# Optimization experiments

Hardware: AMD Instinct MI355X
Metric: run time of the kernel (lower is better)

Reference implementation:

```python
import jax, jax.numpy as jnp
import numpy as np

NORM_EPS = 1e-6


def setup_inputs() -> dict:
    key = jax.random.key(0)
    k1, k2 = jax.random.split(key)
    in_features, out_features = 4096, 4096
    x = jax.random.normal(k1, (2, 2048, in_features), dtype=jnp.float32)
    scale = 1.0 / np.sqrt(in_features)
    weight = jax.random.normal(k2, (out_features, in_features), dtype=jnp.float32) * scale
    norm_weight = jnp.ones((in_features,), dtype=jnp.float32)
    return {"x": x, "weight": weight, "norm_weight": norm_weight}


def reference(x, weight, norm_weight):
    # RMSNorm over the last dim
    rms = jnp.sqrt(jnp.mean(x * x, axis=-1, keepdims=True) + NORM_EPS)
    x_n = x / rms * norm_weight
    # ternary weight quantization (absmean scale alpha)
    alpha = jnp.maximum(jnp.mean(jnp.abs(weight)), 1e-10)
    w_q = jnp.clip(jnp.round(weight / alpha), -1.0, 1.0)
    # per-token int8 activation quantization (absmax scale gamma)
    gamma = jnp.maximum(jnp.max(jnp.abs(x_n), axis=-1, keepdims=True), 1e-10)
    x_q = jnp.clip(jnp.round(x_n * 127.0 / gamma), -128.0, 127.0)
    # rescaled matmul: y = x_q @ w_q.T * (alpha * gamma / 127)
    y = jnp.einsum('bsk,nk->bsn', x_q, w_q) * (alpha * gamma / 127.0)
    return y
```

## Files before the change

### kernel.cpp

```cpp
#include <hip/hip_runtime.h>
#include <cstdint>
#include <cstddef>


#define KD 4096
#define MD 4096
#define ND 4096

typedef int i32x4 __attribute__((ext_vector_type(4)));

__device__ __forceinline__ void gl2lds16(const signed char* g, signed char* l) {
  __builtin_amdgcn_global_load_lds(
      (const __attribute__((address_space(1))) void*)g,
      (__attribute__((address_space(3))) void*)l, 16, 0, 0);
}

__device__ __forceinline__ float wave_sum(float v) {
#pragma unroll
  for (int off = 32; off; off >>= 1) v += __shfl_down(v, off, 64);
  return v;
}
__device__ __forceinline__ float wave_max(float v) {
#pragma unroll
  for (int off = 32; off; off >>= 1) v = fmaxf(v, __shfl_down(v, off, 64));
  return v;
}


__global__ __launch_bounds__(256) void k_alpha_part(const float* __restrict__ w,
                                                    float* __restrict__ part) {
  __shared__ float red[4];
  const int tid = threadIdx.x;
  const float4* w4 = (const float4*)(w + (size_t)blockIdx.x * 4096);
  float s = 0.f;
#pragma unroll
  for (int i = 0; i < 4; ++i) {
    float4 v = w4[i * 256 + tid];
    s += fabsf(v.x) + fabsf(v.y) + fabsf(v.z) + fabsf(v.w);
  }
  s = wave_sum(s);
  if ((tid & 63) == 0) red[tid >> 6] = s;
  __syncthreads();
  if (tid == 0) part[blockIdx.x] = (red[0] + red[1]) + (red[2] + red[3]);
}

__global__ __launch_bounds__(256) void k_alpha_final(const float* __restrict__ part,
                                                     float* __restrict__ alpha) {
  __shared__ float red[4];
  const int tid = threadIdx.x;
  float s = 0.f;
#pragma unroll
  for (int i = 0; i < 16; ++i) s += part[i * 256 + tid];
  s = wave_sum(s);
  if ((tid & 63) == 0) red[tid >> 6] = s;
  __syncthreads();
  if (tid == 0)
    alpha[0] = fmaxf(((red[0] + red[1]) + (red[2] + red[3])) * (1.0f / 16777216.0f),
                     1e-10f);
}


__global__ __launch_bounds__(256) void k_quant_w(const float* __restrict__ w,
                                                 const float* __restrict__ alpha_p,
                                                 signed char* __restrict__ wq) {
  const float alpha = alpha_p[0];
  const int tid = threadIdx.x;
  const float4* w4 = (const float4*)(w + (size_t)blockIdx.x * 4096);
  uint32_t* wqi = (uint32_t*)(wq + (size_t)blockIdx.x * 4096);
#pragma unroll
  for (int i = 0; i < 4; ++i) {
    const int f = i * 256 + tid;
    float4 v = w4[f];
    int q0 = (int)fminf(fmaxf(rintf(v.x / alpha), -1.f), 1.f);
    int q1 = (int)fminf(fmaxf(rintf(v.y / alpha), -1.f), 1.f);
    int q2 = (int)fminf(fmaxf(rintf(v.z / alpha), -1.f), 1.f);
    int q3 = (int)fminf(fmaxf(rintf(v.w / alpha), -1.f), 1.f);
    wqi[f] = (uint32_t)(q0 & 255) | ((uint32_t)(q1 & 255) << 8) |
             ((uint32_t)(q2 & 255) << 16) | ((uint32_t)(q3 & 255) << 24);
  }
}


__global__ __launch_bounds__(256) void k_rmsnorm_quant(const float* __restrict__ x,
                                                       const float* __restrict__ nw,
                                                       signed char* __restrict__ xq,
                                                       float* __restrict__ gamma) {
  __shared__ float red[4];
  __shared__ float red2[4];
  const int tid = threadIdx.x;
  const int row = blockIdx.x;
  const float4* x4 = (const float4*)(x + (size_t)row * 4096);
  const float4* n4 = (const float4*)nw;
  float4 xv[4], nv[4];
  float ss = 0.f;
#pragma unroll
  for (int i = 0; i < 4; ++i) {
    xv[i] = x4[i * 256 + tid];
    nv[i] = n4[i * 256 + tid];
    ss += xv[i].x * xv[i].x + xv[i].y * xv[i].y + xv[i].z * xv[i].z + xv[i].w * xv[i].w;
  }
  ss = wave_sum(ss);
  if ((tid & 63) == 0) red[tid >> 6] = ss;
  __syncthreads();
  const float tot = (red[0] + red[1]) + (red[2] + red[3]);
  const float rms = sqrtf(tot * (1.0f / 4096.0f) + 1e-6f);

  float4 xn[4];
  float mx = 0.f;
#pragma unroll
  for (int i = 0; i < 4; ++i) {
    xn[i].x = xv[i].x / rms * nv[i].x;
    xn[i].y = xv[i].y / rms * nv[i].y;
    xn[i].z = xv[i].z / rms * nv[i].z;
    xn[i].w = xv[i].w / rms * nv[i].w;
    mx = fmaxf(mx, fmaxf(fmaxf(fabsf(xn[i].x), fabsf(xn[i].y)),
                         fmaxf(fabsf(xn[i].z), fabsf(xn[i].w))));
  }
  mx = wave_max(mx);
  if ((tid & 63) == 0) red2[tid >> 6] = mx;
  __syncthreads();
  const float g = fmaxf(fmaxf(fmaxf(red2[0], red2[1]), fmaxf(red2[2], red2[3])),
                        1e-10f);
  if (tid == 0) gamma[row] = g;

  uint32_t* xqi = (uint32_t*)(xq + (size_t)row * 4096);
#pragma unroll
  for (int i = 0; i < 4; ++i) {
    const int f = i * 256 + tid;
    int q0 = (int)fminf(fmaxf(rintf(xn[i].x * 127.0f / g), -128.f), 127.f);
    int q1 = (int)fminf(fmaxf(rintf(xn[i].y * 127.0f / g), -128.f), 127.f);
    int q2 = (int)fminf(fmaxf(rintf(xn[i].z * 127.0f / g), -128.f), 127.f);
    int q3 = (int)fminf(fmaxf(rintf(xn[i].w * 127.0f / g), -128.f), 127.f);
    xqi[f] = (uint32_t)(q0 & 255) | ((uint32_t)(q1 & 255) << 8) |
             ((uint32_t)(q2 & 255) << 16) | ((uint32_t)(q3 & 255) << 24);
  }
}


__global__ __launch_bounds__(256) void k_gemm(const signed char* __restrict__ xq,
                                              const signed char* __restrict__ wq,
                                              const float* __restrict__ gamma,
                                              const float* __restrict__ alpha_p,
                                              float* __restrict__ out) {
  __shared__ __align__(16) signed char As[128 * 64];
  __shared__ __align__(16) signed char Bs[128 * 64];
  const int tid = threadIdx.x;
  const int lane = tid & 63;
  const int wave = tid >> 6;
  const int wm = (wave >> 1) * 64;
  const int wn = (wave & 1) * 64;
  const int quad = lane >> 4;
  const int l16 = lane & 15;
  const int bm = blockIdx.y * 128;
  const int bn = blockIdx.x * 128;

  const signed char* Ag = xq + (size_t)bm * KD;
  const signed char* Bg = wq + (size_t)bn * KD;

  const int srow = wave * 16 + (lane >> 2);
  const int schunk = (lane & 3) ^ ((lane >> 3) & 3);
  const signed char* agp0 = Ag + (size_t)srow * KD + schunk * 16;
  const signed char* agp1 = Ag + (size_t)(srow + 64) * KD + schunk * 16;
  const signed char* bgp0 = Bg + (size_t)srow * KD + schunk * 16;
  const signed char* bgp1 = Bg + (size_t)(srow + 64) * KD + schunk * 16;
  signed char* la0 = &As[wave * 1024];
  signed char* la1 = &As[4096 + wave * 1024];
  signed char* lb0 = &Bs[wave * 1024];
  signed char* lb1 = &Bs[4096 + wave * 1024];

  i32x4 acc[4][4];
#pragma unroll
  for (int i = 0; i < 4; ++i)
#pragma unroll
    for (int j = 0; j < 4; ++j) acc[i][j] = (i32x4){0, 0, 0, 0};

  const int sw = (l16 >> 1) & 3;
  const int apos = (quad ^ sw) * 16;

  for (int k0 = 0; k0 < KD; k0 += 64) {
    __syncthreads();
    gl2lds16(agp0 + k0, la0);
    gl2lds16(agp1 + k0, la1);
    gl2lds16(bgp0 + k0, lb0);
    gl2lds16(bgp1 + k0, lb1);
    __syncthreads();

    i32x4 af[4], bf[4];
#pragma unroll
    for (int mi = 0; mi < 4; ++mi)
      af[mi] = *(const i32x4*)&As[(wm + mi * 16 + l16) * 64 + apos];
#pragma unroll
    for (int ni = 0; ni < 4; ++ni)
      bf[ni] = *(const i32x4*)&Bs[(wn + ni * 16 + l16) * 64 + apos];
#pragma unroll
    for (int mi = 0; mi < 4; ++mi)
#pragma unroll
      for (int ni = 0; ni < 4; ++ni)
        acc[mi][ni] = __builtin_amdgcn_mfma_i32_16x16x64_i8(af[mi], bf[ni],
                                                            acc[mi][ni], 0, 0, 0);
  }

  const float alpha = alpha_p[0];
#pragma unroll
  for (int mi = 0; mi < 4; ++mi) {
#pragma unroll
    for (int r = 0; r < 4; ++r) {
      const int m = bm + wm + mi * 16 + quad * 4 + r;
      const float s = (alpha * gamma[m]) / 127.0f;
#pragma unroll
      for (int ni = 0; ni < 4; ++ni) {
        const int n = bn + wn + ni * 16 + l16;
        out[(size_t)m * ND + n] = (float)acc[mi][ni][r] * s;
      }
    }
  }
}


extern "C" void kernel_launch(void* const* d_in, const int* in_sizes, int n_in,
                              void* d_out, int out_size, void* d_ws, size_t ws_size,
                              hipStream_t stream) {
  const float* x = (const float*)d_in[0];
  const float* w = (const float*)d_in[1];
  const float* nw = (const float*)d_in[2];
  float* out = (float*)d_out;

  char* ws = (char*)d_ws;
  signed char* xq = (signed char*)ws;
  signed char* wq = (signed char*)(ws + ((size_t)1 << 24));
  float* gamma = (float*)(ws + ((size_t)2 << 24));
  float* part = (float*)(ws + ((size_t)2 << 24) + 16384);
  float* alpha = (float*)(ws + ((size_t)2 << 24) + 32768);

  k_alpha_part<<<4096, 256, 0, stream>>>(w, part);
  k_alpha_final<<<1, 256, 0, stream>>>(part, alpha);
  k_quant_w<<<4096, 256, 0, stream>>>(w, alpha, wq);
  k_rmsnorm_quant<<<4096, 256, 0, stream>>>(x, nw, xq, gamma);
  dim3 g(ND / 128, MD / 128);
  k_gemm<<<g, 256, 0, stream>>>(xq, wq, gamma, alpha, out);
}
```

Measured before the change: 269.9 us.

## Fuse alpha finalize and quantize kernels; double GEMM K-tile to 128

Merges the alpha-final, weight-quantize and RMSNorm-quantize kernels into one launch. Each weight block recomputes alpha from the partial sums, and activation rows are handled by the upper half of the grid. This removes two launches and the serial single-block kernel. The GEMM K step grows from 64 to 128 with a new XOR swizzle, halving the barrier-bounded iterations at the cost of doubling LDS per block to 32KB and redundantly reading the partials in every weight block.

```diff
diff --git a/kernel.cpp b/kernel.cpp
--- a/kernel.cpp
+++ b/kernel.cpp
@@ -44,95 +44,93 @@
   if (tid == 0) part[blockIdx.x] = (red[0] + red[1]) + (red[2] + red[3]);
 }
 
-__global__ __launch_bounds__(256) void k_alpha_final(const float* __restrict__ part,
-                                                     float* __restrict__ alpha) {
-  __shared__ float red[4];
+
+__global__ __launch_bounds__(256) void k_quant_all(const float* __restrict__ w,
+                                                   const float* __restrict__ x,
+                                                   const float* __restrict__ nw,
+                                                   const float* __restrict__ part,
+                                                   signed char* __restrict__ wq,
+                                                   signed char* __restrict__ xq,
+                                                   float* __restrict__ gamma,
+                                                   float* __restrict__ alpha_out) {
   const int tid = threadIdx.x;
-  float s = 0.f;
-#pragma unroll
-  for (int i = 0; i < 16; ++i) s += part[i * 256 + tid];
-  s = wave_sum(s);
-  if ((tid & 63) == 0) red[tid >> 6] = s;
-  __syncthreads();
-  if (tid == 0)
-    alpha[0] = fmaxf(((red[0] + red[1]) + (red[2] + red[3])) * (1.0f / 16777216.0f),
-                     1e-10f);
-}
-
-
-__global__ __launch_bounds__(256) void k_quant_w(const float* __restrict__ w,
-                                                 const float* __restrict__ alpha_p,
-                                                 signed char* __restrict__ wq) {
-  const float alpha = alpha_p[0];
-  const int tid = threadIdx.x;
-  const float4* w4 = (const float4*)(w + (size_t)blockIdx.x * 4096);
-  uint32_t* wqi = (uint32_t*)(wq + (size_t)blockIdx.x * 4096);
-#pragma unroll
-  for (int i = 0; i < 4; ++i) {
-    const int f = i * 256 + tid;
-    float4 v = w4[f];
-    int q0 = (int)fminf(fmaxf(rintf(v.x / alpha), -1.f), 1.f);
-    int q1 = (int)fminf(fmaxf(rintf(v.y / alpha), -1.f), 1.f);
-    int q2 = (int)fminf(fmaxf(rintf(v.z / alpha), -1.f), 1.f);
-    int q3 = (int)fminf(fmaxf(rintf(v.w / alpha), -1.f), 1.f);
-    wqi[f] = (uint32_t)(q0 & 255) | ((uint32_t)(q1 & 255) << 8) |
-             ((uint32_t)(q2 & 255) << 16) | ((uint32_t)(q3 & 255) << 24);
-  }
-}
-
-
-__global__ __launch_bounds__(256) void k_rmsnorm_quant(const float* __restrict__ x,
-                                                       const float* __restrict__ nw,
-                                                       signed char* __restrict__ xq,
-                                                       float* __restrict__ gamma) {
+  const int bid = blockIdx.x;
   __shared__ float red[4];
   __shared__ float red2[4];
-  const int tid = threadIdx.x;
-  const int row = blockIdx.x;
-  const float4* x4 = (const float4*)(x + (size_t)row * 4096);
-  const float4* n4 = (const float4*)nw;
-  float4 xv[4], nv[4];
-  float ss = 0.f;
-#pragma unroll
-  for (int i = 0; i < 4; ++i) {
-    xv[i] = x4[i * 256 + tid];
-    nv[i] = n4[i * 256 + tid];
-    ss += xv[i].x * xv[i].x + xv[i].y * xv[i].y + xv[i].z * xv[i].z + xv[i].w * xv[i].w;
-  }
-  ss = wave_sum(ss);
-  if ((tid & 63) == 0) red[tid >> 6] = ss;
-  __syncthreads();
-  const float tot = (red[0] + red[1]) + (red[2] + red[3]);
-  const float rms = sqrtf(tot * (1.0f / 4096.0f) + 1e-6f);
-
-  float4 xn[4];
-  float mx = 0.f;
-#pragma unroll
-  for (int i = 0; i < 4; ++i) {
-    xn[i].x = xv[i].x / rms * nv[i].x;
-    xn[i].y = xv[i].y / rms * nv[i].y;
-    xn[i].z = xv[i].z / rms * nv[i].z;
-    xn[i].w = xv[i].w / rms * nv[i].w;
-    mx = fmaxf(mx, fmaxf(fmaxf(fabsf(xn[i].x), fabsf(xn[i].y)),
-                         fmaxf(fabsf(xn[i].z), fabsf(xn[i].w))));
-  }
-  mx = wave_max(mx);
-  if ((tid & 63) == 0) red2[tid >> 6] = mx;
-  __syncthreads();
-  const float g = fmaxf(fmaxf(fmaxf(red2[0], red2[1]), fmaxf(red2[2], red2[3])),
-                        1e-10f);
-  if (tid == 0) gamma[row] = g;
-
-  uint32_t* xqi = (uint32_t*)(xq + (size_t)row * 4096);
-#pragma unroll
-  for (int i = 0; i < 4; ++i) {
-    const int f = i * 256 + tid;
-    int q0 = (int)fminf(fmaxf(rintf(xn[i].x * 127.0f / g), -128.f), 127.f);
-    int q1 = (int)fminf(fmaxf(rintf(xn[i].y * 127.0f / g), -128.f), 127.f);
-    int q2 = (int)fminf(fmaxf(rintf(xn[i].z * 127.0f / g), -128.f), 127.f);
-    int q3 = (int)fminf(fmaxf(rintf(xn[i].w * 127.0f / g), -128.f), 127.f);
-    xqi[f] = (uint32_t)(q0 & 255) | ((uint32_t)(q1 & 255) << 8) |
-             ((uint32_t)(q2 & 255) << 16) | ((uint32_t)(q3 & 255) << 24);
+
+  if (bid < 4096) {
+    float s = 0.f;
+#pragma unroll
+    for (int i = 0; i < 16; ++i) s += part[i * 256 + tid];
+    s = wave_sum(s);
+    if ((tid & 63) == 0) red[tid >> 6] = s;
+    __syncthreads();
+    const float alpha =
+        fmaxf(((red[0] + red[1]) + (red[2] + red[3])) * (1.0f / 16777216.0f),
+              1e-10f);
+    if (bid == 0 && tid == 0) alpha_out[0] = alpha;
+
+    const float4* w4 = (const float4*)(w + (size_t)bid * 4096);
+    uint32_t* wqi = (uint32_t*)(wq + (size_t)bid * 4096);
+#pragma unroll
+    for (int i = 0; i < 4; ++i) {
+      const int f = i * 256 + tid;
+      float4 v = w4[f];
+      int q0 = (int)fminf(fmaxf(rintf(v.x / alpha), -1.f), 1.f);
+      int q1 = (int)fminf(fmaxf(rintf(v.y / alpha), -1.f), 1.f);
+      int q2 = (int)fminf(fmaxf(rintf(v.z / alpha), -1.f), 1.f);
+      int q3 = (int)fminf(fmaxf(rintf(v.w / alpha), -1.f), 1.f);
+      wqi[f] = (uint32_t)(q0 & 255) | ((uint32_t)(q1 & 255) << 8) |
+               ((uint32_t)(q2 & 255) << 16) | ((uint32_t)(q3 & 255) << 24);
+    }
+  } else {
+    const int row = bid - 4096;
+    const float4* x4 = (const float4*)(x + (size_t)row * 4096);
+    const float4* n4 = (const float4*)nw;
+    float4 xv[4], nv[4];
+    float ss = 0.f;
+#pragma unroll
+    for (int i = 0; i < 4; ++i) {
+      xv[i] = x4[i * 256 + tid];
+      nv[i] = n4[i * 256 + tid];
+      ss += xv[i].x * xv[i].x + xv[i].y * xv[i].y + xv[i].z * xv[i].z +
+            xv[i].w * xv[i].w;
+    }
+    ss = wave_sum(ss);
+    if ((tid & 63) == 0) red[tid >> 6] = ss;
+    __syncthreads();
+    const float tot = (red[0] + red[1]) + (red[2] + red[3]);
+    const float rms = sqrtf(tot * (1.0f / 4096.0f) + 1e-6f);
+
+    float4 xn[4];
+    float mx = 0.f;
+#pragma unroll
+    for (int i = 0; i < 4; ++i) {
+      xn[i].x = xv[i].x / rms * nv[i].x;
+      xn[i].y = xv[i].y / rms * nv[i].y;
+      xn[i].z = xv[i].z / rms * nv[i].z;
+      xn[i].w = xv[i].w / rms * nv[i].w;
+      mx = fmaxf(mx, fmaxf(fmaxf(fabsf(xn[i].x), fabsf(xn[i].y)),
+                           fmaxf(fabsf(xn[i].z), fabsf(xn[i].w))));
+    }
+    mx = wave_max(mx);
+    if ((tid & 63) == 0) red2[tid >> 6] = mx;
+    __syncthreads();
+    const float g = fmaxf(
+        fmaxf(fmaxf(red2[0], red2[1]), fmaxf(red2[2], red2[3])), 1e-10f);
+    if (tid == 0) gamma[row] = g;
+
+    uint32_t* xqi = (uint32_t*)(xq + (size_t)row * 4096);
+#pragma unroll
+    for (int i = 0; i < 4; ++i) {
+      const int f = i * 256 + tid;
+      int q0 = (int)fminf(fmaxf(rintf(xn[i].x * 127.0f / g), -128.f), 127.f);
+      int q1 = (int)fminf(fmaxf(rintf(xn[i].y * 127.0f / g), -128.f), 127.f);
+      int q2 = (int)fminf(fmaxf(rintf(xn[i].z * 127.0f / g), -128.f), 127.f);
+      int q3 = (int)fminf(fmaxf(rintf(xn[i].w * 127.0f / g), -128.f), 127.f);
+      xqi[f] = (uint32_t)(q0 & 255) | ((uint32_t)(q1 & 255) << 8) |
+               ((uint32_t)(q2 & 255) << 16) | ((uint32_t)(q3 & 255) << 24);
+    }
   }
 }
 
@@ -142,8 +140,8 @@
                                               const float* __restrict__ gamma,
                                               const float* __restrict__ alpha_p,
                                               float* __restrict__ out) {
-  __shared__ __align__(16) signed char As[128 * 64];
-  __shared__ __align__(16) signed char Bs[128 * 64];
+  __shared__ __align__(16) signed char As[128 * 128];
+  __shared__ __align__(16) signed char Bs[128 * 128];
   const int tid = threadIdx.x;
   const int lane = tid & 63;
   const int wave = tid >> 6;
@@ -157,16 +155,20 @@
   const signed char* Ag = xq + (size_t)bm * KD;
   const signed char* Bg = wq + (size_t)bn * KD;
 
-  const int srow = wave * 16 + (lane >> 2);
-  const int schunk = (lane & 3) ^ ((lane >> 3) & 3);
-  const signed char* agp0 = Ag + (size_t)srow * KD + schunk * 16;
-  const signed char* agp1 = Ag + (size_t)(srow + 64) * KD + schunk * 16;
-  const signed char* bgp0 = Bg + (size_t)srow * KD + schunk * 16;
-  const signed char* bgp1 = Bg + (size_t)(srow + 64) * KD + schunk * 16;
-  signed char* la0 = &As[wave * 1024];
-  signed char* la1 = &As[4096 + wave * 1024];
-  signed char* lb0 = &Bs[wave * 1024];
-  signed char* lb1 = &Bs[4096 + wave * 1024];
+  const int lr = lane >> 3;
+  const int sc = (lane & 7) ^ lr;
+  const signed char* agp[4];
+  const signed char* bgp[4];
+  signed char* la[4];
+  signed char* lb[4];
+#pragma unroll
+  for (int i = 0; i < 4; ++i) {
+    const int R = i * 32 + wave * 8 + lr;
+    agp[i] = Ag + (size_t)R * KD + sc * 16;
+    bgp[i] = Bg + (size_t)R * KD + sc * 16;
+    la[i] = &As[(i * 32 + wave * 8) * 128];
+    lb[i] = &Bs[(i * 32 + wave * 8) * 128];
+  }
 
   i32x4 acc[4][4];
 #pragma unroll
@@ -174,30 +176,33 @@
 #pragma unroll
     for (int j = 0; j < 4; ++j) acc[i][j] = (i32x4){0, 0, 0, 0};
 
-  const int sw = (l16 >> 1) & 3;
-  const int apos = (quad ^ sw) * 16;
-
-  for (int k0 = 0; k0 < KD; k0 += 64) {
-    __syncthreads();
-    gl2lds16(agp0 + k0, la0);
-    gl2lds16(agp1 + k0, la1);
-    gl2lds16(bgp0 + k0, lb0);
-    gl2lds16(bgp1 + k0, lb1);
-    __syncthreads();
-
-    i32x4 af[4], bf[4];
-#pragma unroll
-    for (int mi = 0; mi < 4; ++mi)
-      af[mi] = *(const i32x4*)&As[(wm + mi * 16 + l16) * 64 + apos];
-#pragma unroll
-    for (int ni = 0; ni < 4; ++ni)
-      bf[ni] = *(const i32x4*)&Bs[(wn + ni * 16 + l16) * 64 + apos];
-#pragma unroll
-    for (int mi = 0; mi < 4; ++mi)
+  const int swz = l16 & 7;
+
+  for (int k0 = 0; k0 < KD; k0 += 128) {
+    __syncthreads();
+#pragma unroll
+    for (int i = 0; i < 4; ++i) gl2lds16(agp[i] + k0, la[i]);
+#pragma unroll
+    for (int i = 0; i < 4; ++i) gl2lds16(bgp[i] + k0, lb[i]);
+    __syncthreads();
+
+#pragma unroll
+    for (int ks = 0; ks < 2; ++ks) {
+      const int pos = ((ks * 4 + quad) ^ swz) * 16;
+      i32x4 af[4], bf[4];
+#pragma unroll
+      for (int mi = 0; mi < 4; ++mi)
+        af[mi] = *(const i32x4*)&As[(wm + mi * 16 + l16) * 128 + pos];
 #pragma unroll
       for (int ni = 0; ni < 4; ++ni)
-        acc[mi][ni] = __builtin_amdgcn_mfma_i32_16x16x64_i8(af[mi], bf[ni],
-                                                            acc[mi][ni], 0, 0, 0);
+        bf[ni] = *(const i32x4*)&Bs[(wn + ni * 16 + l16) * 128 + pos];
+#pragma unroll
+      for (int mi = 0; mi < 4; ++mi)
+#pragma unroll
+        for (int ni = 0; ni < 4; ++ni)
+          acc[mi][ni] = __builtin_amdgcn_mfma_i32_16x16x64_i8(af[mi], bf[ni],
+                                                              acc[mi][ni], 0, 0, 0);
+    }
   }
 
   const float alpha = alpha_p[0];
@@ -233,9 +238,7 @@
   float* alpha = (float*)(ws + ((size_t)2 << 24) + 32768);
 
   k_alpha_part<<<4096, 256, 0, stream>>>(w, part);
-  k_alpha_final<<<1, 256, 0, stream>>>(part, alpha);
-  k_quant_w<<<4096, 256, 0, stream>>>(w, alpha, wq);
-  k_rmsnorm_quant<<<4096, 256, 0, stream>>>(x, nw, xq, gamma);
+  k_quant_all<<<8192, 256, 0, stream>>>(w, x, nw, part, wq, xq, gamma, alpha);
   dim3 g(ND / 128, MD / 128);
   k_gemm<<<g, 256, 0, stream>>>(xq, wq, gamma, alpha, out);
 }
```

After: 244.1 us. 1.11x faster.
